# Kernel tuning notes

Measured on AMD Instinct MI355X. Metric: run time of the kernel, lower is better.

## Reference

```python
import jax, jax.numpy as jnp
import numpy as np
import math

SCALING = math.sqrt(3.0)

def setup_inputs() -> dict:
    key = jax.random.key(0)
    ks = jax.random.split(key, 5)
    B, S, I, H = 32, 1024, 1024, 1024
    std = math.sqrt(3.0 / (3 * H))
    x = jax.random.normal(ks[0], (B, S, I), dtype=jnp.float32)
    w = jax.random.uniform(ks[1], (3 * H, I), dtype=jnp.float32, minval=-std, maxval=std)
    b = jax.random.normal(ks[2], (3 * H,), dtype=jnp.float32) * 0.01
    v_f = jax.random.normal(ks[3], (H,), dtype=jnp.float32) * 0.1
    v_r = jax.random.normal(ks[4], (H,), dtype=jnp.float32) * 0.1
    return {"x": x, "w": w, "b": b, "v_f": v_f, "v_r": v_r}

def reference(x, w, b, v_f, v_r):
    B, S, I = x.shape
    H = v_f.shape[0]
    # big GEMM: [B,S,I] x [I,3H] -> [B,S,3H]
    wx = jnp.einsum('bsi,hi->bsh', x, w) + b
    wf_x = wx[..., :H]
    wc_x = wx[..., H:2 * H]
    wr_x = wx[..., 2 * H:]
    c0 = jnp.zeros((B, H), dtype=x.dtype)

    def step(c, inp):
        wf_t, wc_t = inp  # each [B,H]
        f = jax.nn.sigmoid(wf_t + v_f * c)
        c_new = f * (c - wc_t) + wc_t
        return c_new, (c, c_new)  # (prev_c, c) per step

    # scan over time: transpose to [S,B,H]
    _, (prev_cs, cs) = jax.lax.scan(
        step, c0, (jnp.swapaxes(wf_x, 0, 1), jnp.swapaxes(wc_x, 0, 1)))
    prev_cs = jnp.swapaxes(prev_cs, 0, 1)  # [B,S,H]
    cs = jnp.swapaxes(cs, 0, 1)            # [B,S,H]

    r = jax.nn.sigmoid(wr_x + v_r * prev_cs)
    xs = x * SCALING
    h = r * (cs - xs) + xs
    return h, cs[:, -1]
```

## Files before the change

### kernel.cpp

```cpp
#include <hip/hip_runtime.h>

typedef unsigned short u16;
typedef unsigned int u32;
typedef __attribute__((ext_vector_type(4))) float f32x4;
typedef __attribute__((ext_vector_type(4))) u16 u16x4;
typedef __attribute__((ext_vector_type(8))) __bf16 bf16x8;

#define BDIM 32
#define SDIM 1024
#define HDIM 1024
#define MT (BDIM*SDIM)
#define NT (3*HDIM)
#define KT 1024

__device__ __forceinline__ float bf2f(u16 u) {
  u32 x = ((u32)u) << 16;
  return __builtin_bit_cast(float, x);
}
__device__ __forceinline__ u16 f2bf(float f) {
  u32 x = __builtin_bit_cast(u32, f);
  x = x + 0x7fffu + ((x >> 16) & 1u);
  return (u16)(x >> 16);
}

typedef __attribute__((address_space(1))) void gvoid;
typedef __attribute__((address_space(3))) void lvoid;
__device__ __forceinline__ void gload16(const u16* g, u16* l) {
  __builtin_amdgcn_global_load_lds((gvoid*)g, (lvoid*)l, 16, 0, 0);
}

__global__ void cast_kernel(const float* __restrict__ in, u16* __restrict__ out, int n4) {
  int idx = blockIdx.x * blockDim.x + threadIdx.x;
  int stride = gridDim.x * blockDim.x;
  const f32x4* in4 = (const f32x4*)in;
  u16x4* out4 = (u16x4*)out;
  for (int i = idx; i < n4; i += stride) {
    f32x4 v = in4[i];
    u16x4 o;
    o[0] = f2bf(v[0]); o[1] = f2bf(v[1]); o[2] = f2bf(v[2]); o[3] = f2bf(v[3]);
    out4[i] = o;
  }
}

__global__ __launch_bounds__(256) void gemm_kernel(
    const u16* __restrict__ A,
    const u16* __restrict__ W,
    const float* __restrict__ bias,
    u16* __restrict__ C)
{
  __shared__ u16 As[128 * 32];
  __shared__ u16 Bs[128 * 32];
  const int tid  = threadIdx.x;
  const int lane = tid & 63;
  const int wave = tid >> 6;

  int bid = blockIdx.x;
  bid = (bid & 7) * 768 + (bid >> 3);
  const int bm = bid / (NT / 128);
  const int bn = bid % (NT / 128);
  const int wm = (wave >> 1) * 64;
  const int wn = (wave & 1) * 64;

  f32x4 acc[4][4] = {};

  const int rsub = lane >> 2;
  const int ksub = (lane & 3) * 8;
  const int c0 = wave * 2;

  const u16* Ab0 = A + (size_t)(bm * 128 + c0 * 16 + rsub) * KT + ksub;
  const u16* Ab1 = A + (size_t)(bm * 128 + (c0 + 1) * 16 + rsub) * KT + ksub;
  const u16* Wb0 = W + (size_t)(bn * 128 + c0 * 16 + rsub) * KT + ksub;
  const u16* Wb1 = W + (size_t)(bn * 128 + (c0 + 1) * 16 + rsub) * KT + ksub;
  u16* lA0 = &As[c0 * 512];
  u16* lA1 = &As[(c0 + 1) * 512];
  u16* lB0 = &Bs[c0 * 512];
  u16* lB1 = &Bs[(c0 + 1) * 512];

  const int fr = lane & 15;
  const int fk = (lane >> 4) * 8;

  for (int kt = 0; kt < KT / 32; ++kt) {
    const int k0 = kt * 32;
    gload16(Ab0 + k0, lA0);
    gload16(Ab1 + k0, lA1);
    gload16(Wb0 + k0, lB0);
    gload16(Wb1 + k0, lB1);
    __syncthreads();

    bf16x8 av[4], bv[4];
#pragma unroll
    for (int mi = 0; mi < 4; ++mi)
      av[mi] = *(const bf16x8*)&As[(wm + mi * 16 + fr) * 32 + fk];
#pragma unroll
    for (int ni = 0; ni < 4; ++ni)
      bv[ni] = *(const bf16x8*)&Bs[(wn + ni * 16 + fr) * 32 + fk];
#pragma unroll
    for (int mi = 0; mi < 4; ++mi)
#pragma unroll
      for (int ni = 0; ni < 4; ++ni)
        acc[mi][ni] = __builtin_amdgcn_mfma_f32_16x16x32_bf16(av[mi], bv[ni], acc[mi][ni], 0, 0, 0);
    __syncthreads();
  }

  const int crow  = bm * 128 + wm + (lane >> 4) * 4;
  const int ccol0 = bn * 128 + wn + (lane & 15);
#pragma unroll
  for (int ni = 0; ni < 4; ++ni) {
    const int col = ccol0 + ni * 16;
    const float bb = bias[col];
#pragma unroll
    for (int mi = 0; mi < 4; ++mi) {
#pragma unroll
      for (int v = 0; v < 4; ++v) {
        C[(size_t)(crow + mi * 16 + v) * NT + col] = f2bf(acc[mi][ni][v] + bb);
      }
    }
  }
}

__global__ __launch_bounds__(64) void scan_kernel(
    const u16* __restrict__ wx,
    const float* __restrict__ x,
    const float* __restrict__ vf,
    const float* __restrict__ vr,
    float* __restrict__ h_out,
    float* __restrict__ c_last)
{
  const int lane = threadIdx.x;
  const int bid  = blockIdx.x;
  const int b    = bid >> 4;
  const int h    = ((bid & 15) << 6) + lane;

  const float vfh = vf[h];
  const float vrh = vr[h];
  const float SC = 1.7320508075688772f;

  const u16* pw = wx + (size_t)b * SDIM * NT + h;
  const float* px = x + (size_t)b * SDIM * HDIM + h;
  float* ph = h_out + (size_t)b * SDIM * HDIM + h;

  float c = 0.0f;
#pragma unroll 8
  for (int t = 0; t < SDIM; ++t) {
    const float wf = bf2f(pw[0]);
    const float wc = bf2f(pw[HDIM]);
    const float wr = bf2f(pw[2 * HDIM]);
    const float xv = px[0];

    const float ef = __expf(-(wf + vfh * c));
    const float f  = 1.0f / (1.0f + ef);
    const float cn = f * (c - wc) + wc;

    const float er = __expf(-(wr + vrh * c));
    const float r  = 1.0f / (1.0f + er);

    const float xs = xv * SC;
    ph[0] = r * (cn - xs) + xs;

    c = cn;
    pw += NT; px += HDIM; ph += HDIM;
  }
  c_last[(size_t)b * HDIM + h] = c;
}

extern "C" void kernel_launch(void* const* d_in, const int* in_sizes, int n_in,
                              void* d_out, int out_size, void* d_ws, size_t ws_size,
                              hipStream_t stream) {
  const float* x  = (const float*)d_in[0];
  const float* w  = (const float*)d_in[1];
  const float* b  = (const float*)d_in[2];
  const float* vf = (const float*)d_in[3];
  const float* vr = (const float*)d_in[4];

  float* out    = (float*)d_out;
  float* h_out  = out;
  float* c_last = out + (size_t)33554432;

  char* ws = (char*)d_ws;
  u16* xb = (u16*)ws;
  u16* wb = (u16*)(ws + 67108864);
  u16* wx = (u16*)(ws + 67108864 + 6291456);

  cast_kernel<<<4096, 256, 0, stream>>>(x, xb, (int)(33554432 / 4));
  cast_kernel<<<1024, 256, 0, stream>>>(w, wb, (int)(3145728 / 4));
  gemm_kernel<<<(MT / 128) * (NT / 128), 256, 0, stream>>>(xb, wb, b, wx);
  scan_kernel<<<512, 64, 0, stream>>>(wx, x, vf, vr, h_out, c_last);
}
```

Baseline: 649.2 us.

## Prefetch scan inputs in chunks via registers into double-buffered LDS

The recurrent scan kernel is restructured to load 16-timestep chunks of the gate pre-activations and input with 16-byte vector loads into registers. Each chunk is staged into a double-buffered shared-memory tile while the previous chunk is computed, so the serial recurrence no longer waits on scattered 2-byte global loads each step. It also reads the bf16 copy of x already produced for the GEMM instead of the fp32 original, which halves that traffic. The cost is a precision loss in the residual x term of the output.

```diff
diff --git a/kernel.cpp b/kernel.cpp
--- a/kernel.cpp
+++ b/kernel.cpp
@@ -4,6 +4,7 @@
 typedef unsigned int u32;
 typedef __attribute__((ext_vector_type(4))) float f32x4;
 typedef __attribute__((ext_vector_type(4))) u16 u16x4;
+typedef __attribute__((ext_vector_type(8))) u16 u16x8;
 typedef __attribute__((ext_vector_type(8))) __bf16 bf16x8;
 
 #define BDIM 32
@@ -118,48 +119,91 @@
   }
 }
 
+#define CH 16
+#define NCH (SDIM/CH)
 __global__ __launch_bounds__(64) void scan_kernel(
     const u16* __restrict__ wx,
-    const float* __restrict__ x,
+    const u16* __restrict__ xb,
     const float* __restrict__ vf,
     const float* __restrict__ vr,
     float* __restrict__ h_out,
     float* __restrict__ c_last)
 {
+  __shared__ u16 smem[2][4][CH * 64];
   const int lane = threadIdx.x;
   const int bid  = blockIdx.x;
   const int b    = bid >> 4;
-  const int h    = ((bid & 15) << 6) + lane;
+  const int h0   = (bid & 15) << 6;
+  const int h    = h0 + lane;
 
   const float vfh = vf[h];
   const float vrh = vr[h];
   const float SC = 1.7320508075688772f;
 
-  const u16* pw = wx + (size_t)b * SDIM * NT + h;
-  const float* px = x + (size_t)b * SDIM * HDIM + h;
-  float* ph = h_out + (size_t)b * SDIM * HDIM + h;
+  const int lrow = lane >> 3;
+  const int lcol = (lane & 7) * 8;
+  const u16* wxb = wx + (size_t)(b * SDIM) * NT + h0 + lcol;
+  const u16* xbb = xb + (size_t)(b * SDIM) * HDIM + h0 + lcol;
+
+  float* ph = h_out + (size_t)(b * SDIM) * HDIM + h;
+
+  u16x8 rg[4][2];
+
+  auto load_chunk = [&](int t0) {
+#pragma unroll
+    for (int j = 0; j < 2; ++j) {
+      const size_t m = (size_t)(t0 + j * 8 + lrow);
+      rg[0][j] = *(const u16x8*)(wxb + m * NT);
+      rg[1][j] = *(const u16x8*)(wxb + m * NT + HDIM);
+      rg[2][j] = *(const u16x8*)(wxb + m * NT + 2 * HDIM);
+      rg[3][j] = *(const u16x8*)(xbb + m * HDIM);
+    }
+  };
+  auto write_chunk = [&](int buf) {
+#pragma unroll
+    for (int a = 0; a < 4; ++a)
+#pragma unroll
+      for (int j = 0; j < 2; ++j)
+        *(u16x8*)&smem[buf][a][j * 512 + lane * 8] = rg[a][j];
+  };
 
   float c = 0.0f;
-#pragma unroll 8
-  for (int t = 0; t < SDIM; ++t) {
-    const float wf = bf2f(pw[0]);
-    const float wc = bf2f(pw[HDIM]);
-    const float wr = bf2f(pw[2 * HDIM]);
-    const float xv = px[0];
-
-    const float ef = __expf(-(wf + vfh * c));
-    const float f  = 1.0f / (1.0f + ef);
-    const float cn = f * (c - wc) + wc;
-
-    const float er = __expf(-(wr + vrh * c));
-    const float r  = 1.0f / (1.0f + er);
-
-    const float xs = xv * SC;
-    ph[0] = r * (cn - xs) + xs;
-
-    c = cn;
-    pw += NT; px += HDIM; ph += HDIM;
-  }
+
+  auto compute_chunk = [&](int k, int buf) {
+    const u16* sf = &smem[buf][0][lane];
+    const u16* sw = &smem[buf][1][lane];
+    const u16* sr = &smem[buf][2][lane];
+    const u16* sx = &smem[buf][3][lane];
+    const int t0 = k * CH;
+#pragma unroll
+    for (int r = 0; r < CH; ++r) {
+      const float wf = bf2f(sf[r * 64]);
+      const float wc = bf2f(sw[r * 64]);
+      const float wr = bf2f(sr[r * 64]);
+      const float xv = bf2f(sx[r * 64]);
+
+      const float ef = __expf(-(wf + vfh * c));
+      const float f  = 1.0f / (1.0f + ef);
+      const float cn = f * (c - wc) + wc;
+
+      const float er = __expf(-(wr + vrh * c));
+      const float rr = 1.0f / (1.0f + er);
+
+      const float xs = xv * SC;
+      ph[(size_t)(t0 + r) * HDIM] = rr * (cn - xs) + xs;
+      c = cn;
+    }
+  };
+
+  load_chunk(0);
+  write_chunk(0);
+  for (int k = 0; k < NCH - 1; ++k) {
+    load_chunk((k + 1) * CH);
+    compute_chunk(k, k & 1);
+    write_chunk((k + 1) & 1);
+  }
+  compute_chunk(NCH - 1, (NCH - 1) & 1);
+
   c_last[(size_t)b * HDIM + h] = c;
 }
 
@@ -184,5 +228,5 @@
   cast_kernel<<<4096, 256, 0, stream>>>(x, xb, (int)(33554432 / 4));
   cast_kernel<<<1024, 256, 0, stream>>>(w, wb, (int)(3145728 / 4));
   gemm_kernel<<<(MT / 128) * (NT / 128), 256, 0, stream>>>(xb, wb, b, wx);
-  scan_kernel<<<512, 64, 0, stream>>>(wx, x, vf, vr, h_out, c_last);
-}
+  scan_kernel<<<512, 64, 0, stream>>>(wx, xb, vf, vr, h_out, c_last);
+}
```

Result: faster. 619.2 us (-4.6%).

## Store GEMM output in gate-major time-packed layout and prefetch scan inputs in chunks

Applied to the files above, without the earlier changes.

The GEMM epilogue now writes each gate into its own region, packing four consecutive time steps per lane as a u16x4 and laying data out per (batch, hidden-group) block. Each scan thread can then fetch 8-byte vectors covering four steps instead of scalar 2-byte loads strided by 3H. The scan loop is restructured to software-prefetch 16-step chunks across four register buffers, so loads for later chunks are in flight while the serial recurrence runs on the current one. This targets the latency-bound serial scan. The cost is more register pressure from the buffers and a less coalesced GEMM epilogue store pattern.

```diff
diff --git a/kernel.cpp b/kernel.cpp
--- a/kernel.cpp
+++ b/kernel.cpp
@@ -4,6 +4,7 @@
 typedef unsigned int u32;
 typedef __attribute__((ext_vector_type(4))) float f32x4;
 typedef __attribute__((ext_vector_type(4))) u16 u16x4;
+typedef __attribute__((ext_vector_type(8))) u16 u16x8;
 typedef __attribute__((ext_vector_type(8))) __bf16 bf16x8;
 
 #define BDIM 32
@@ -12,6 +13,7 @@
 #define MT (BDIM*SDIM)
 #define NT (3*HDIM)
 #define KT 1024
+#define GATE_U16X4 8388608u
 
 __device__ __forceinline__ float bf2f(u16 u) {
   u32 x = ((u32)u) << 16;
@@ -46,7 +48,7 @@
     const u16* __restrict__ A,
     const u16* __restrict__ W,
     const float* __restrict__ bias,
-    u16* __restrict__ C)
+    u16x4* __restrict__ CT)
 {
   __shared__ u16 As[128 * 32];
   __shared__ u16 Bs[128 * 32];
@@ -102,24 +104,36 @@
     __syncthreads();
   }
 
-  const int crow  = bm * 128 + wm + (lane >> 4) * 4;
-  const int ccol0 = bn * 128 + wn + (lane & 15);
+  const int b_i   = bm >> 3;
+  const int trow  = ((bm & 7) << 7) + wm + ((lane >> 4) << 2);
+  const int g     = bn >> 3;
+  const int hbase = ((bn & 7) << 7) + wn + (lane & 15);
+  u16x4* Tg = CT + (size_t)g * GATE_U16X4;
+
 #pragma unroll
   for (int ni = 0; ni < 4; ++ni) {
-    const int col = ccol0 + ni * 16;
-    const float bb = bias[col];
+    const int h  = hbase + ni * 16;
+    const int hg = h >> 6;
+    const int hl = h & 63;
+    const float bb = bias[g * 1024 + h];
 #pragma unroll
     for (int mi = 0; mi < 4; ++mi) {
-#pragma unroll
-      for (int v = 0; v < 4; ++v) {
-        C[(size_t)(crow + mi * 16 + v) * NT + col] = f2bf(acc[mi][ni][v] + bb);
-      }
+      const int t4 = (trow + mi * 16) >> 2;
+      u16x4 o;
+#pragma unroll
+      for (int v = 0; v < 4; ++v) o[v] = f2bf(acc[mi][ni][v] + bb);
+      Tg[((size_t)(b_i * 16 + hg) * 256 + t4) * 64 + hl] = o;
     }
   }
 }
 
+struct Buf {
+  u16x4 f[4], w[4], r[4];
+  float x[16];
+};
+
 __global__ __launch_bounds__(64) void scan_kernel(
-    const u16* __restrict__ wx,
+    const u16x4* __restrict__ CT,
     const float* __restrict__ x,
     const float* __restrict__ vf,
     const float* __restrict__ vr,
@@ -129,37 +143,68 @@
   const int lane = threadIdx.x;
   const int bid  = blockIdx.x;
   const int b    = bid >> 4;
-  const int h    = ((bid & 15) << 6) + lane;
+  const int hg   = bid & 15;
+  const int h    = (hg << 6) + lane;
 
   const float vfh = vf[h];
   const float vrh = vr[h];
   const float SC = 1.7320508075688772f;
 
-  const u16* pw = wx + (size_t)b * SDIM * NT + h;
-  const float* px = x + (size_t)b * SDIM * HDIM + h;
-  float* ph = h_out + (size_t)b * SDIM * HDIM + h;
+  const u16x4* Tf = CT + (size_t)(b * 16 + hg) * 256 * 64 + lane;
+  const u16x4* Tw = Tf + GATE_U16X4;
+  const u16x4* Tr = Tf + 2 * (size_t)GATE_U16X4;
+  const float* px = x + (size_t)(b * SDIM) * HDIM + h;
+  float* ph = h_out + (size_t)(b * SDIM) * HDIM + h;
+
+  auto LOAD = [&](Buf& bf, int kc) {
+#pragma unroll
+    for (int j = 0; j < 4; ++j) {
+      const size_t o = (size_t)(kc * 4 + j) * 64;
+      bf.f[j] = Tf[o];
+      bf.w[j] = Tw[o];
+      bf.r[j] = Tr[o];
+    }
+#pragma unroll
+    for (int r = 0; r < 16; ++r)
+      bf.x[r] = px[(size_t)(kc * 16 + r) * HDIM];
+  };
 
   float c = 0.0f;
-#pragma unroll 8
-  for (int t = 0; t < SDIM; ++t) {
-    const float wf = bf2f(pw[0]);
-    const float wc = bf2f(pw[HDIM]);
-    const float wr = bf2f(pw[2 * HDIM]);
-    const float xv = px[0];
-
-    const float ef = __expf(-(wf + vfh * c));
-    const float f  = 1.0f / (1.0f + ef);
-    const float cn = f * (c - wc) + wc;
-
-    const float er = __expf(-(wr + vrh * c));
-    const float r  = 1.0f / (1.0f + er);
-
-    const float xs = xv * SC;
-    ph[0] = r * (cn - xs) + xs;
-
-    c = cn;
-    pw += NT; px += HDIM; ph += HDIM;
-  }
+
+  auto COMPUTE = [&](const Buf& bf, int k) {
+#pragma unroll
+    for (int r = 0; r < 16; ++r) {
+      const float wf = bf2f(bf.f[r >> 2][r & 3]);
+      const float wc = bf2f(bf.w[r >> 2][r & 3]);
+      const float wr = bf2f(bf.r[r >> 2][r & 3]);
+      const float xv = bf.x[r];
+
+      const float ef = __expf(-(wf + vfh * c));
+      const float fg = 1.0f / (1.0f + ef);
+      const float cn = fg * (c - wc) + wc;
+
+      const float er = __expf(-(wr + vrh * c));
+      const float rr = 1.0f / (1.0f + er);
+
+      const float xs = xv * SC;
+      ph[(size_t)(k * 16 + r) * HDIM] = rr * (cn - xs) + xs;
+      c = cn;
+    }
+  };
+
+  Buf A0, A1, B0, B1;
+  LOAD(A0, 0); LOAD(A1, 1);
+  for (int k = 0; k < 64; k += 4) {
+    LOAD(B0, (k + 2 < 64) ? k + 2 : 63);
+    COMPUTE(A0, k);
+    LOAD(B1, (k + 3 < 64) ? k + 3 : 63);
+    COMPUTE(A1, k + 1);
+    LOAD(A0, (k + 4 < 64) ? k + 4 : 63);
+    COMPUTE(B0, k + 2);
+    LOAD(A1, (k + 5 < 64) ? k + 5 : 63);
+    COMPUTE(B1, k + 3);
+  }
+
   c_last[(size_t)b * HDIM + h] = c;
 }
 
@@ -179,10 +224,10 @@
   char* ws = (char*)d_ws;
   u16* xb = (u16*)ws;
   u16* wb = (u16*)(ws + 67108864);
-  u16* wx = (u16*)(ws + 67108864 + 6291456);
+  u16x4* wxT = (u16x4*)(ws + 67108864 + 6291456);
 
   cast_kernel<<<4096, 256, 0, stream>>>(x, xb, (int)(33554432 / 4));
   cast_kernel<<<1024, 256, 0, stream>>>(w, wb, (int)(3145728 / 4));
-  gemm_kernel<<<(MT / 128) * (NT / 128), 256, 0, stream>>>(xb, wb, b, wx);
-  scan_kernel<<<512, 64, 0, stream>>>(wx, x, vf, vr, h_out, c_last);
-}
+  gemm_kernel<<<(MT / 128) * (NT / 128), 256, 0, stream>>>(xb, wb, b, wxT);
+  scan_kernel<<<512, 64, 0, stream>>>(wxT, x, vf, vr, h_out, c_last);
+}
```

Result: faster. 626.3 us (-3.5%).

## Split scan into serial c-recurrence and parallel output pass with tiled wx layout

Applied to the files above, without the earlier changes.

The GEMM epilogue now writes wx in a tiled layout: the f and c gates are interleaved as packed 4-timestep vectors per (batch, h-group) block, and the r gate goes to a separate buffer. The serial scan kernel now reads only the f/c gates with an 8-deep register prefetch ring and writes bf16 c values. A second, fully parallel kernel computes the r gate and the output h from those stored c values. This moves most memory traffic and the r/x work off the latency-bound 512-block recurrence. In exchange it adds an extra pass over c and stores c in bf16, which loses precision in the h output.

```diff
diff --git a/kernel.cpp b/kernel.cpp
--- a/kernel.cpp
+++ b/kernel.cpp
@@ -4,6 +4,7 @@
 typedef unsigned int u32;
 typedef __attribute__((ext_vector_type(4))) float f32x4;
 typedef __attribute__((ext_vector_type(4))) u16 u16x4;
+typedef __attribute__((ext_vector_type(8))) u16 u16x8;
 typedef __attribute__((ext_vector_type(8))) __bf16 bf16x8;
 
 #define BDIM 32
@@ -12,6 +13,7 @@
 #define MT (BDIM*SDIM)
 #define NT (3*HDIM)
 #define KT 1024
+#define TILE_U (8388608u)
 
 __device__ __forceinline__ float bf2f(u16 u) {
   u32 x = ((u32)u) << 16;
@@ -46,7 +48,8 @@
     const u16* __restrict__ A,
     const u16* __restrict__ W,
     const float* __restrict__ bias,
-    u16* __restrict__ C)
+    u16x4* __restrict__ PW,
+    u16x4* __restrict__ R)
 {
   __shared__ u16 As[128 * 32];
   __shared__ u16 Bs[128 * 32];
@@ -102,65 +105,104 @@
     __syncthreads();
   }
 
-  const int crow  = bm * 128 + wm + (lane >> 4) * 4;
-  const int ccol0 = bn * 128 + wn + (lane & 15);
+  const int b_i   = bm >> 3;
+  const int trow  = ((bm & 7) << 7) + wm + ((lane >> 4) << 2);
+  const int g     = bn >> 3;
+  const int hbase = ((bn & 7) << 7) + wn + (lane & 15);
+
 #pragma unroll
   for (int ni = 0; ni < 4; ++ni) {
-    const int col = ccol0 + ni * 16;
-    const float bb = bias[col];
+    const int h  = hbase + ni * 16;
+    const int hg = h >> 6;
+    const int hl = h & 63;
+    const float bb = bias[g * 1024 + h];
 #pragma unroll
     for (int mi = 0; mi < 4; ++mi) {
-#pragma unroll
-      for (int v = 0; v < 4; ++v) {
-        C[(size_t)(crow + mi * 16 + v) * NT + col] = f2bf(acc[mi][ni][v] + bb);
-      }
+      const int t4 = (trow + mi * 16) >> 2;
+      const size_t idx = ((size_t)(b_i * 16 + hg) * 256 + t4) * 64 + hl;
+      u16x4 o;
+#pragma unroll
+      for (int v = 0; v < 4; ++v) o[v] = f2bf(acc[mi][ni][v] + bb);
+      if (g < 2) PW[idx * 2 + g] = o;
+      else       R[idx] = o;
     }
   }
 }
 
-__global__ __launch_bounds__(64) void scan_kernel(
-    const u16* __restrict__ wx,
-    const float* __restrict__ x,
+__global__ __launch_bounds__(64) void scan1_kernel(
+    const u16x8* __restrict__ PW,
     const float* __restrict__ vf,
-    const float* __restrict__ vr,
-    float* __restrict__ h_out,
+    u16x4* __restrict__ Cc,
     float* __restrict__ c_last)
 {
   const int lane = threadIdx.x;
-  const int bid  = blockIdx.x;
-  const int b    = bid >> 4;
-  const int h    = ((bid & 15) << 6) + lane;
+  const int bhg  = blockIdx.x;
+  const int b    = bhg >> 4;
+  const int h    = ((bhg & 15) << 6) + lane;
 
   const float vfh = vf[h];
+  const u16x8* base = PW + (size_t)bhg * 256 * 64 + lane;
+  u16x4* cw = Cc + (size_t)bhg * 256 * 64 + lane;
+
+  u16x8 ring[8];
+#pragma unroll
+  for (int j = 0; j < 8; ++j) ring[j] = base[(size_t)j * 64];
+
+  float c = 0.0f;
+#pragma unroll 8
+  for (int g = 0; g < 256; ++g) {
+    const u16x8 cur = ring[g & 7];
+    const int gp = (g + 8 < 256) ? (g + 8) : 255;
+    ring[g & 7] = base[(size_t)gp * 64];
+    u16x4 oc;
+#pragma unroll
+    for (int v = 0; v < 4; ++v) {
+      const float wf = bf2f(cur[v]);
+      const float wc = bf2f(cur[4 + v]);
+      const float ef = __expf(-(wf + vfh * c));
+      const float f  = 1.0f / (1.0f + ef);
+      c = f * (c - wc) + wc;
+      oc[v] = f2bf(c);
+    }
+    cw[(size_t)g * 64] = oc;
+  }
+  c_last[(size_t)b * HDIM + h] = c;
+}
+
+__global__ __launch_bounds__(256) void scan2_kernel(
+    const u16x4* __restrict__ R,
+    const u16x4* __restrict__ Cc,
+    const float* __restrict__ x,
+    const float* __restrict__ vr,
+    float* __restrict__ h_out)
+{
+  const int tid = threadIdx.x;
+  const int blk = blockIdx.x;
+  const int bhg = blk >> 6;
+  const int t4  = ((blk & 63) << 2) + (tid >> 6);
+  const int hl  = tid & 63;
+  const int b   = bhg >> 4;
+  const int h   = ((bhg & 15) << 6) + hl;
+
+  const size_t idx = ((size_t)bhg * 256 + t4) * 64 + hl;
+  const u16x4 r4 = R[idx];
+  const u16x4 c4 = Cc[idx];
+  const size_t idxp = (t4 == 0) ? idx : idx - 64;
+  const float cprev = (t4 == 0) ? 0.0f : bf2f(Cc[idxp][3]);
   const float vrh = vr[h];
   const float SC = 1.7320508075688772f;
 
-  const u16* pw = wx + (size_t)b * SDIM * NT + h;
-  const float* px = x + (size_t)b * SDIM * HDIM + h;
-  float* ph = h_out + (size_t)b * SDIM * HDIM + h;
-
-  float c = 0.0f;
-#pragma unroll 8
-  for (int t = 0; t < SDIM; ++t) {
-    const float wf = bf2f(pw[0]);
-    const float wc = bf2f(pw[HDIM]);
-    const float wr = bf2f(pw[2 * HDIM]);
-    const float xv = px[0];
-
-    const float ef = __expf(-(wf + vfh * c));
-    const float f  = 1.0f / (1.0f + ef);
-    const float cn = f * (c - wc) + wc;
-
-    const float er = __expf(-(wr + vrh * c));
-    const float r  = 1.0f / (1.0f + er);
-
-    const float xs = xv * SC;
-    ph[0] = r * (cn - xs) + xs;
-
-    c = cn;
-    pw += NT; px += HDIM; ph += HDIM;
-  }
-  c_last[(size_t)b * HDIM + h] = c;
+  const float* px = x + ((size_t)b * SDIM + t4 * 4) * HDIM + h;
+  float* ph = h_out + ((size_t)b * SDIM + t4 * 4) * HDIM + h;
+
+#pragma unroll
+  for (int v = 0; v < 4; ++v) {
+    const float cp = (v == 0) ? cprev : bf2f(c4[v - 1]);
+    const float er = __expf(-(bf2f(r4[v]) + vrh * cp));
+    const float rr = 1.0f / (1.0f + er);
+    const float xs = px[(size_t)v * HDIM] * SC;
+    ph[(size_t)v * HDIM] = rr * (bf2f(c4[v]) - xs) + xs;
+  }
 }
 
 extern "C" void kernel_launch(void* const* d_in, const int* in_sizes, int n_in,
@@ -177,12 +219,15 @@
   float* c_last = out + (size_t)33554432;
 
   char* ws = (char*)d_ws;
-  u16* xb = (u16*)ws;
-  u16* wb = (u16*)(ws + 67108864);
-  u16* wx = (u16*)(ws + 67108864 + 6291456);
-
-  cast_kernel<<<4096, 256, 0, stream>>>(x, xb, (int)(33554432 / 4));
-  cast_kernel<<<1024, 256, 0, stream>>>(w, wb, (int)(3145728 / 4));
-  gemm_kernel<<<(MT / 128) * (NT / 128), 256, 0, stream>>>(xb, wb, b, wx);
-  scan_kernel<<<512, 64, 0, stream>>>(wx, x, vf, vr, h_out, c_last);
-}
+  u16*   xb = (u16*)ws;
+  u16*   wb = (u16*)(ws + 67108864);
+  u16x4* PW = (u16x4*)(ws + 73400320);
+  u16x4* R  = (u16x4*)(ws + 73400320 + 134217728);
+  u16x4* Cc = (u16x4*)ws;
+
+  cast_kernel<<<4096, 256, 0, stream>>>(x, xb, 8388608);
+  cast_kernel<<<1024, 256, 0, stream>>>(w, wb, 786432);
+  gemm_kernel<<<(MT / 128) * (NT / 128), 256, 0, stream>>>(xb, wb, b, PW, R);
+  scan1_kernel<<<512, 64, 0, stream>>>((const u16x8*)PW, vf, Cc, c_last);
+  scan2_kernel<<<32768, 256, 0, stream>>>(R, Cc, x, vr, h_out);
+}
```

Result: faster. 612.6 us (-5.6%).
